# Kernel tuning notes

Hardware: AMD Instinct MI355X
Metric: run time of the kernel (lower is better)

The kernel has to match this reference:

```python
import jax, jax.numpy as jnp
import numpy as np

V, H, NTYPES = 32000, 2048, 55
B, S = 4, 4096
SPANS_PER_ITEM = 512
LN_EPS = 1e-5


def _layernorm(x, g, b):
    m = jnp.mean(x, axis=-1, keepdims=True)
    v = jnp.mean(jnp.square(x - m), axis=-1, keepdims=True)
    return (x - m) * jax.lax.rsqrt(v + LN_EPS) * g + b


def setup_inputs() -> dict:
    key = jax.random.key(0)
    ks = jax.random.split(key, 16)
    inp = {
        'input_ids': jax.random.randint(ks[0], (B, S), 0, V, dtype=jnp.int64),
        'span_ids': jax.random.randint(ks[1], (B, S), 0, SPANS_PER_ITEM, dtype=jnp.int32),
        'span_type_ids': jax.random.randint(ks[2], (B * SPANS_PER_ITEM,), 0, NTYPES, dtype=jnp.int32),
        # learned params
        'tok_table': jax.random.normal(ks[3], (V, H), jnp.float32) * 0.02,
        'W1': jax.random.normal(ks[4], (H, H), jnp.float32) * 0.02,
        'b1': jnp.zeros((H,), jnp.float32),
        'W2': jax.random.normal(ks[5], (H, H), jnp.float32) * 0.02,
        'b2': jnp.zeros((H,), jnp.float32),
        'type_table': jax.random.normal(ks[6], (NTYPES, H), jnp.float32) * 0.02,
        'Wp': jax.random.normal(ks[7], (H, H), jnp.float32) * 0.02,
        'bp': jnp.zeros((H,), jnp.float32),
        'ln_g': jnp.ones((H,), jnp.float32),
        'ln_b': jnp.zeros((H,), jnp.float32),
        'Wg': jax.random.normal(ks[8], (2 * H, H), jnp.float32) * 0.02,
        'bg': jnp.zeros((H,), jnp.float32),
    }
    return inp


def reference(input_ids, span_ids, span_type_ids, tok_table, W1, b1, W2, b2,
              type_table, Wp, bp, ln_g, ln_b, Wg, bg):
    Bq, Sq = input_ids.shape
    num_spans = span_type_ids.shape[0]
    spans_per_item = num_spans // Bq

    # token embeddings + residual adapter: x + Linear(GELU(Linear(x)))
    tok = tok_table[input_ids]                                   # [B,S,H]
    tok = tok + jax.nn.gelu(tok @ W1 + b1, approximate=False) @ W2 + b2

    # ragged per-span mean pool (spans are per-batch-item -> offset ids)
    seg = (span_ids + jnp.arange(Bq, dtype=span_ids.dtype)[:, None] * spans_per_item).reshape(-1)
    flat = tok.reshape(-1, tok.shape[-1])                        # [B*S,H]
    sums = jax.ops.segment_sum(flat, seg, num_segments=num_spans)
    cnt = jax.ops.segment_sum(jnp.ones((flat.shape[0],), flat.dtype), seg, num_segments=num_spans)
    pooled = sums / jnp.maximum(cnt, 1.0)[:, None]               # [num_spans,H]

    # add span-type embedding, project
    enhanced = (pooled + type_table[span_type_ids]) @ Wp + bp    # [num_spans,H]

    # spans with <=1 tokens are skipped (mask=0, keep token emb)
    valid = cnt > 1.0                                            # [num_spans]
    tok_valid = valid[seg]                                       # [B*S]
    span_emb = jnp.where(tok_valid[:, None], enhanced[seg], flat).reshape(tok.shape)
    span_mask = tok_valid.astype(tok.dtype).reshape(Bq, Sq)

    span_emb_norm = _layernorm(span_emb, ln_g, ln_b)
    gate = jax.nn.sigmoid(jnp.concatenate([tok, span_emb_norm], axis=-1) @ Wg + bg)
    gate = gate * span_mask[..., None]
    combined = (1.0 - gate) * tok + gate * span_emb              # dropout = identity (eval)
    return combined, gate, span_mask
```

## Files before the change

### kernel.cpp

```cpp
#include <hip/hip_runtime.h>
#include <stdint.h>

#define H 2048
#define BTOK 16384
#define NSEG 2048
#define SPANS 512
#define SEQ 4096

typedef __attribute__((ext_vector_type(8))) short bf16x8;
typedef __attribute__((ext_vector_type(4))) float f32x4;

__device__ __forceinline__ short f2bf(float f) {
  union { float f; uint32_t u; } x; x.f = f;
  uint32_t r = x.u + 0x7FFFu + ((x.u >> 16) & 1u);
  return (short)(uint16_t)(r >> 16);
}
__device__ __forceinline__ float bf2f(short h) {
  union { uint32_t u; float f; } x; x.u = ((uint32_t)(uint16_t)h) << 16;
  return x.f;
}

typedef __attribute__((address_space(1))) const void* gas_t;
typedef __attribute__((address_space(3))) void* las_t;
__device__ __forceinline__ void stage16(const void* g, void* l) {
  __builtin_amdgcn_global_load_lds((gas_t)g, (las_t)l, 16, 0, 0);
}

__global__ void detect_ids_kernel(const void* __restrict__ ids, int* __restrict__ flag) {
  __shared__ int any;
  if (threadIdx.x == 0) any = 0;
  __syncthreads();
  const long long* p = (const long long*)ids;
  int bad = 0;
  for (int i = threadIdx.x; i < 8192; i += 256) {
    long long v = p[i];
    if (v < 0 || v >= 32000) bad = 1;
  }
  if (bad) any = 1;
  __syncthreads();
  if (threadIdx.x == 0) flag[0] = any;
}

__global__ void ids_norm_kernel(const void* __restrict__ ids, const int* __restrict__ flag,
                                int* __restrict__ ids32) {
  int i = blockIdx.x * 256 + threadIdx.x;
  if (flag[0]) {
    ids32[i] = ((const int*)ids)[i];
  } else {
    ids32[i] = (int)((const long long*)ids)[i];
  }
}

__global__ __launch_bounds__(256) void wconv_kernel(const float* __restrict__ W,
                                                    short* __restrict__ Wt, int K, int N) {
  __shared__ float t[32][33];
  int nt = N >> 5;
  int ti = blockIdx.x / nt;
  int tj = blockIdx.x % nt;
  int x = threadIdx.x & 31;
  int y = threadIdx.x >> 5;
  #pragma unroll
  for (int yy = 0; yy < 32; yy += 8)
    t[yy + y][x] = W[(size_t)(ti * 32 + yy + y) * N + tj * 32 + x];
  __syncthreads();
  #pragma unroll
  for (int yy = 0; yy < 32; yy += 8)
    Wt[(size_t)(tj * 32 + yy + y) * K + ti * 32 + x] = f2bf(t[x][yy + y]);
}

__global__ __launch_bounds__(256) void embed_kernel(const int* __restrict__ ids32,
                                                    const float* __restrict__ table,
                                                    short* __restrict__ emb) {
  int m = blockIdx.x;
  int row = ids32[m];
  const float4* src = (const float4*)(table + (size_t)row * H) + threadIdx.x * 2;
  float4 a = src[0], b = src[1];
  bf16x8 o;
  o[0] = f2bf(a.x); o[1] = f2bf(a.y); o[2] = f2bf(a.z); o[3] = f2bf(a.w);
  o[4] = f2bf(b.x); o[5] = f2bf(b.y); o[6] = f2bf(b.z); o[7] = f2bf(b.w);
  *(bf16x8*)(emb + (size_t)m * H + threadIdx.x * 8) = o;
}

#define BM 128
#define BN 128
#define BK 32

template<int EPI>
__global__ __launch_bounds__(256, 2) void gemm_kernel(
    const short* __restrict__ A, const short* __restrict__ A2, int K1,
    const short* __restrict__ Bt, const float* __restrict__ bias,
    int M, int N, int K,
    const short* __restrict__ embres, short* __restrict__ outb,
    const int* __restrict__ span_ids, const int* __restrict__ valid,
    const short* __restrict__ tokp, const short* __restrict__ enh,
    float* __restrict__ outC, float* __restrict__ outG) {
  __shared__ __align__(16) short lA[BM * BK];
  __shared__ __align__(16) short lB[BN * BK];
  const int tid = threadIdx.x;
  const int wave = tid >> 6;
  const int lane = tid & 63;
  const int MB = M / BM;
  const int nwg = gridDim.x;
  const int cpx = nwg >> 3;
  const int swz = (blockIdx.x & 7) * cpx + (blockIdx.x >> 3);
  const int bm = swz % MB;
  const int bn = swz / MB;
  const int wm = wave >> 1, wn = wave & 1;

  f32x4 zero4 = {0.f, 0.f, 0.f, 0.f};
  f32x4 acc[4][4];
  #pragma unroll
  for (int i = 0; i < 4; ++i)
    #pragma unroll
    for (int j = 0; j < 4; ++j) acc[i][j] = zero4;

  const int sr = wave * 32 + (lane >> 2);
  const int kc = (lane & 3) * 8;
  const int ar0 = bm * BM + sr;
  const int br0 = bn * BN + sr;
  short* ldsA0 = &lA[(wave * 32) * BK];
  short* ldsA1 = &lA[(wave * 32 + 16) * BK];
  short* ldsB0 = &lB[(wave * 32) * BK];
  short* ldsB1 = &lB[(wave * 32 + 16) * BK];

  const int clr = lane & 15;
  const int clk = (lane >> 4) * 8;

  for (int kk = 0; kk < K; kk += BK) {
    const short* Ab; int ko, as_;
    if (kk < K1) { Ab = A; ko = kk; as_ = K1; }
    else         { Ab = A2; ko = kk - K1; as_ = K - K1; }
    __syncthreads();
    stage16(Ab + (size_t)ar0 * as_ + ko + kc, ldsA0);
    stage16(Ab + (size_t)(ar0 + 16) * as_ + ko + kc, ldsA1);
    stage16(Bt + (size_t)br0 * K + kk + kc, ldsB0);
    stage16(Bt + (size_t)(br0 + 16) * K + kk + kc, ldsB1);
    __syncthreads();

    bf16x8 af[4], bfr[4];
    #pragma unroll
    for (int mi = 0; mi < 4; ++mi)
      af[mi] = *(const bf16x8*)&lA[(wm * 64 + mi * 16 + clr) * BK + clk];
    #pragma unroll
    for (int ni = 0; ni < 4; ++ni)
      bfr[ni] = *(const bf16x8*)&lB[(wn * 64 + ni * 16 + clr) * BK + clk];
    #pragma unroll
    for (int mi = 0; mi < 4; ++mi)
      #pragma unroll
      for (int ni = 0; ni < 4; ++ni)
        acc[mi][ni] = __builtin_amdgcn_mfma_f32_16x16x32_bf16(af[mi], bfr[ni], acc[mi][ni], 0, 0, 0);
  }

  const int lg = lane >> 4;
  const int rb = bm * BM + wm * 64;
  const int cb = bn * BN + wn * 64;
  #pragma unroll
  for (int ni = 0; ni < 4; ++ni) {
    const int c = cb + ni * 16 + clr;
    const float bv = bias[c];
    #pragma unroll
    for (int mi = 0; mi < 4; ++mi) {
      const int r0e = rb + mi * 16 + lg * 4;
      #pragma unroll
      for (int j = 0; j < 4; ++j) {
        const int r = r0e + j;
        float x = acc[mi][ni][j] + bv;
        if (EPI == 0) {
          float g = 0.5f * x * (1.f + erff(x * 0.70710678118654752f));
          outb[(size_t)r * N + c] = f2bf(g);
        } else if (EPI == 1) {
          x += bf2f(embres[(size_t)r * N + c]);
          outb[(size_t)r * N + c] = f2bf(x);
        } else if (EPI == 2) {
          outb[(size_t)r * N + c] = f2bf(x);
        } else {
          const int seg = ((r >> 12) << 9) + span_ids[r];
          const int v = valid[seg];
          const float g = v ? (1.f / (1.f + __expf(-x))) : 0.f;
          const float te = bf2f(tokp[(size_t)r * H + c]);
          const float se = v ? bf2f(enh[(size_t)seg * H + c]) : te;
          outC[(size_t)r * H + c] = (1.f - g) * te + g * se;
          outG[(size_t)r * H + c] = g;
        }
      }
    }
  }
}

__global__ __launch_bounds__(256) void pool_kernel(
    const short* __restrict__ tok, const int* __restrict__ span_ids,
    const int* __restrict__ span_type_ids, const float* __restrict__ type_table,
    short* __restrict__ pooled, int* __restrict__ valid) {
  __shared__ int list[SEQ];
  __shared__ int nmatch;
  const int gseg = blockIdx.x;
  const int b = gseg >> 9;
  const int sp = gseg & 511;
  if (threadIdx.x == 0) nmatch = 0;
  __syncthreads();
  const int* sid = span_ids + b * SEQ;
  for (int s = threadIdx.x; s < SEQ; s += 256)
    if (sid[s] == sp) list[atomicAdd(&nmatch, 1)] = s;
  __syncthreads();
  const int n = nmatch;
  float accv[8] = {0, 0, 0, 0, 0, 0, 0, 0};
  const int d0 = threadIdx.x * 8;
  for (int i = 0; i < n; ++i) {
    const int s = list[i];
    bf16x8 v = *(const bf16x8*)(tok + ((size_t)(b * SEQ + s)) * H + d0);
    #pragma unroll
    for (int j = 0; j < 8; ++j) accv[j] += bf2f(v[j]);
  }
  const float inv = 1.f / (float)(n > 0 ? n : 1);
  const int t = span_type_ids[gseg];
  const float* tt = type_table + (size_t)t * H + d0;
  bf16x8 o;
  #pragma unroll
  for (int j = 0; j < 8; ++j) o[j] = f2bf(accv[j] * inv + tt[j]);
  *(bf16x8*)(pooled + (size_t)gseg * H + d0) = o;
  if (threadIdx.x == 0) valid[gseg] = (n > 1) ? 1 : 0;
}

__global__ __launch_bounds__(256) void ln_kernel(
    const short* __restrict__ tok, const short* __restrict__ enh,
    const int* __restrict__ span_ids, const int* __restrict__ valid,
    const float* __restrict__ ln_g, const float* __restrict__ ln_b,
    short* __restrict__ normout, float* __restrict__ maskout) {
  const int m = blockIdx.x;
  const int b = m >> 12;
  const int seg = (b << 9) + span_ids[m];
  const int v = valid[seg];
  const short* src = v ? (enh + (size_t)seg * H) : (tok + (size_t)m * H);
  const int d0 = threadIdx.x * 8;
  bf16x8 raw = *(const bf16x8*)(src + d0);
  float vals[8];
  float s = 0.f, s2 = 0.f;
  #pragma unroll
  for (int j = 0; j < 8; ++j) { float f = bf2f(raw[j]); vals[j] = f; s += f; s2 += f * f; }
  #pragma unroll
  for (int o = 32; o > 0; o >>= 1) { s += __shfl_down(s, o); s2 += __shfl_down(s2, o); }
  __shared__ float red[8];
  const int wv = threadIdx.x >> 6, ln = threadIdx.x & 63;
  if (ln == 0) { red[wv] = s; red[4 + wv] = s2; }
  __syncthreads();
  const float S = red[0] + red[1] + red[2] + red[3];
  const float S2 = red[4] + red[5] + red[6] + red[7];
  const float mean = S * (1.f / H);
  const float var = S2 * (1.f / H) - mean * mean;
  const float rstd = rsqrtf(var + 1e-5f);
  const float4* gp = (const float4*)(ln_g + d0);
  const float4* bp = (const float4*)(ln_b + d0);
  float4 g0 = gp[0], g1 = gp[1], b0 = bp[0], b1 = bp[1];
  const float gs[8] = {g0.x, g0.y, g0.z, g0.w, g1.x, g1.y, g1.z, g1.w};
  const float bs[8] = {b0.x, b0.y, b0.z, b0.w, b1.x, b1.y, b1.z, b1.w};
  bf16x8 o;
  #pragma unroll
  for (int j = 0; j < 8; ++j) o[j] = f2bf((vals[j] - mean) * rstd * gs[j] + bs[j]);
  *(bf16x8*)(normout + (size_t)m * H + d0) = o;
  if (threadIdx.x == 0) maskout[m] = v ? 1.f : 0.f;
}

extern "C" void kernel_launch(void* const* d_in, const int* in_sizes, int n_in,
                              void* d_out, int out_size, void* d_ws, size_t ws_size,
                              hipStream_t stream) {
  const void* input_ids = d_in[0];
  const int* span_ids = (const int*)d_in[1];
  const int* span_type_ids = (const int*)d_in[2];
  const float* tok_table = (const float*)d_in[3];
  const float* W1 = (const float*)d_in[4];
  const float* b1 = (const float*)d_in[5];
  const float* W2 = (const float*)d_in[6];
  const float* b2 = (const float*)d_in[7];
  const float* type_table = (const float*)d_in[8];
  const float* Wp = (const float*)d_in[9];
  const float* bp = (const float*)d_in[10];
  const float* ln_g = (const float*)d_in[11];
  const float* ln_b = (const float*)d_in[12];
  const float* Wg = (const float*)d_in[13];
  const float* bg = (const float*)d_in[14];

  char* ws = (char*)d_ws;
  size_t off = 0;
  auto alloc = [&](size_t bytes) -> void* {
    void* p = ws + off;
    off += (bytes + 255) & ~(size_t)255;
    return p;
  };
  short* emb = (short*)alloc((size_t)BTOK * H * 2);
  short* h1 = (short*)alloc((size_t)BTOK * H * 2);
  short* tokb = (short*)alloc((size_t)BTOK * H * 2);
  short* W1t = (short*)alloc((size_t)H * H * 2);
  short* W2t = (short*)alloc((size_t)H * H * 2);
  short* Wpt = (short*)alloc((size_t)H * H * 2);
  short* Wgt = (short*)alloc((size_t)2 * H * H * 2);
  short* pooledA = (short*)alloc((size_t)NSEG * H * 2);
  short* enh = (short*)alloc((size_t)NSEG * H * 2);
  int* validf = (int*)alloc(NSEG * 4);
  int* ids32 = (int*)alloc(BTOK * 4);
  int* flag = (int*)alloc(256);

  float* outC = (float*)d_out;
  float* outG = outC + (size_t)BTOK * H;
  float* outM = outG + (size_t)BTOK * H;

  detect_ids_kernel<<<1, 256, 0, stream>>>(input_ids, flag);
  ids_norm_kernel<<<BTOK / 256, 256, 0, stream>>>(input_ids, flag, ids32);
  wconv_kernel<<<(H / 32) * (H / 32), 256, 0, stream>>>(W1, W1t, H, H);
  wconv_kernel<<<(H / 32) * (H / 32), 256, 0, stream>>>(W2, W2t, H, H);
  wconv_kernel<<<(H / 32) * (H / 32), 256, 0, stream>>>(Wp, Wpt, H, H);
  wconv_kernel<<<(2 * H / 32) * (H / 32), 256, 0, stream>>>(Wg, Wgt, 2 * H, H);
  embed_kernel<<<BTOK, 256, 0, stream>>>(ids32, tok_table, emb);

  gemm_kernel<0><<<(BTOK / BM) * (H / BN), 256, 0, stream>>>(
      emb, emb, H, W1t, b1, BTOK, H, H,
      nullptr, h1, nullptr, nullptr, nullptr, nullptr, nullptr, nullptr);
  gemm_kernel<1><<<(BTOK / BM) * (H / BN), 256, 0, stream>>>(
      h1, h1, H, W2t, b2, BTOK, H, H,
      emb, tokb, nullptr, nullptr, nullptr, nullptr, nullptr, nullptr);
  pool_kernel<<<NSEG, 256, 0, stream>>>(tokb, span_ids, span_type_ids, type_table,
                                        pooledA, validf);
  gemm_kernel<2><<<(NSEG / BM) * (H / BN), 256, 0, stream>>>(
      pooledA, pooledA, H, Wpt, bp, NSEG, H, H,
      nullptr, enh, nullptr, nullptr, nullptr, nullptr, nullptr, nullptr);
  ln_kernel<<<BTOK, 256, 0, stream>>>(tokb, enh, span_ids, validf, ln_g, ln_b, h1, outM);
  gemm_kernel<3><<<(BTOK / BM) * (H / BN), 256, 0, stream>>>(
      tokb, h1, H, Wgt, bg, BTOK, H, 2 * H,
      nullptr, nullptr, span_ids, validf, tokb, enh, outC, outG);
}
```

Baseline: 1.544 ms.

## Double-buffer LDS tiles in GEMM and switch tile order to row-major

The GEMM main loop now uses two LDS buffers, so the global-to-LDS stage for the next K-slice is issued before the MFMA compute on the current slice, with one barrier per iteration instead of two. Block-to-tile mapping also changes from column-major (bm = swz % MB) to row-major (bn = swz % NB), which changes which tiles share A or B in cache. The cost is double the LDS footprint (32KB per block), which may affect the 2-blocks-per-CU occupancy target, and an altered L2 reuse pattern.

```diff
diff --git a/kernel.cpp b/kernel.cpp
--- a/kernel.cpp
+++ b/kernel.cpp
@@ -94,17 +94,18 @@
     const int* __restrict__ span_ids, const int* __restrict__ valid,
     const short* __restrict__ tokp, const short* __restrict__ enh,
     float* __restrict__ outC, float* __restrict__ outG) {
-  __shared__ __align__(16) short lA[BM * BK];
-  __shared__ __align__(16) short lB[BN * BK];
+  __shared__ __align__(16) short lA[2][BM * BK];
+  __shared__ __align__(16) short lB[2][BN * BK];
   const int tid = threadIdx.x;
   const int wave = tid >> 6;
   const int lane = tid & 63;
   const int MB = M / BM;
+  const int NB = N / BN;
   const int nwg = gridDim.x;
   const int cpx = nwg >> 3;
   const int swz = (blockIdx.x & 7) * cpx + (blockIdx.x >> 3);
-  const int bm = swz % MB;
-  const int bn = swz / MB;
+  const int bm = swz / NB;
+  const int bn = swz % NB;
   const int wm = wave >> 1, wn = wave & 1;
 
   f32x4 zero4 = {0.f, 0.f, 0.f, 0.f};
@@ -118,38 +119,44 @@
   const int kc = (lane & 3) * 8;
   const int ar0 = bm * BM + sr;
   const int br0 = bn * BN + sr;
-  short* ldsA0 = &lA[(wave * 32) * BK];
-  short* ldsA1 = &lA[(wave * 32 + 16) * BK];
-  short* ldsB0 = &lB[(wave * 32) * BK];
-  short* ldsB1 = &lB[(wave * 32 + 16) * BK];
 
   const int clr = lane & 15;
   const int clk = (lane >> 4) * 8;
 
-  for (int kk = 0; kk < K; kk += BK) {
+  auto STAGE = [&](int buf, int kk) {
     const short* Ab; int ko, as_;
     if (kk < K1) { Ab = A; ko = kk; as_ = K1; }
     else         { Ab = A2; ko = kk - K1; as_ = K - K1; }
-    __syncthreads();
-    stage16(Ab + (size_t)ar0 * as_ + ko + kc, ldsA0);
-    stage16(Ab + (size_t)(ar0 + 16) * as_ + ko + kc, ldsA1);
-    stage16(Bt + (size_t)br0 * K + kk + kc, ldsB0);
-    stage16(Bt + (size_t)(br0 + 16) * K + kk + kc, ldsB1);
-    __syncthreads();
-
+    stage16(Ab + (size_t)ar0 * as_ + ko + kc, &lA[buf][(wave * 32) * BK]);
+    stage16(Ab + (size_t)(ar0 + 16) * as_ + ko + kc, &lA[buf][(wave * 32 + 16) * BK]);
+    stage16(Bt + (size_t)br0 * K + kk + kc, &lB[buf][(wave * 32) * BK]);
+    stage16(Bt + (size_t)(br0 + 16) * K + kk + kc, &lB[buf][(wave * 32 + 16) * BK]);
+  };
+  auto COMPUTE = [&](int buf) {
     bf16x8 af[4], bfr[4];
     #pragma unroll
     for (int mi = 0; mi < 4; ++mi)
-      af[mi] = *(const bf16x8*)&lA[(wm * 64 + mi * 16 + clr) * BK + clk];
+      af[mi] = *(const bf16x8*)&lA[buf][(wm * 64 + mi * 16 + clr) * BK + clk];
     #pragma unroll
     for (int ni = 0; ni < 4; ++ni)
-      bfr[ni] = *(const bf16x8*)&lB[(wn * 64 + ni * 16 + clr) * BK + clk];
+      bfr[ni] = *(const bf16x8*)&lB[buf][(wn * 64 + ni * 16 + clr) * BK + clk];
     #pragma unroll
     for (int mi = 0; mi < 4; ++mi)
       #pragma unroll
       for (int ni = 0; ni < 4; ++ni)
         acc[mi][ni] = __builtin_amdgcn_mfma_f32_16x16x32_bf16(af[mi], bfr[ni], acc[mi][ni], 0, 0, 0);
-  }
+  };
+
+  STAGE(0, 0);
+  __syncthreads();
+  int cur = 0;
+  for (int kk = BK; kk < K; kk += BK) {
+    STAGE(cur ^ 1, kk);
+    COMPUTE(cur);
+    __syncthreads();
+    cur ^= 1;
+  }
+  COMPUTE(cur);
 
   const int lg = lane >> 4;
   const int rb = bm * BM + wm * 64;
```

Result: no change. 1.538 ms (-0.4%).
